# Performance work log

Measured on AMD Instinct MI355X. Metric: run time of the kernel, lower is better.

## Reference

```python
import jax, jax.numpy as jnp
import numpy as np

DIM = 256
H = 56
W = 56
WS = 7          # window_size
SHIFT = 3       # shift_size = WS // 2
NH = 8          # num_heads
HID = 4 * DIM   # mlp hidden
EPS = 1e-5
N = WS * WS     # tokens per window


def _rel_coords_table():
    # SwinV2 continuous log-spaced relative coords, pretrained_window_size=0
    r = np.arange(-(WS - 1), WS, dtype=np.float32)
    t = np.stack(np.meshgrid(r, r, indexing='ij'), axis=-1)[None]  # (1, 2WS-1, 2WS-1, 2)
    t = t / (WS - 1) * 8.0
    t = np.sign(t) * np.log2(np.abs(t) + 1.0) / np.log2(8.0)
    return jnp.asarray(t, jnp.float32)


def _rel_pos_index():
    coords = np.stack(np.meshgrid(np.arange(WS), np.arange(WS), indexing='ij'))  # (2, WS, WS)
    cf = coords.reshape(2, -1)
    rel = (cf[:, :, None] - cf[:, None, :]).transpose(1, 2, 0).astype(np.int64)  # (N, N, 2)
    rel[..., 0] += WS - 1
    rel[..., 1] += WS - 1
    rel[..., 0] *= 2 * WS - 1
    return jnp.asarray(rel.sum(-1), jnp.int32)  # (N, N)


def _attn_mask():
    # shifted-window mask: -100 where tokens come from different image regions
    img = np.zeros((1, H, W, 1), np.float32)
    cnt = 0
    for hs in (slice(0, -WS), slice(-WS, -SHIFT), slice(-SHIFT, None)):
        for ws_ in (slice(0, -WS), slice(-WS, -SHIFT), slice(-SHIFT, None)):
            img[:, hs, ws_, :] = cnt
            cnt += 1
    mw = img.reshape(1, H // WS, WS, W // WS, WS, 1).transpose(0, 1, 3, 2, 4, 5).reshape(-1, N)
    m = mw[:, None, :] - mw[:, :, None]
    return jnp.asarray(np.where(m != 0, -100.0, 0.0).astype(np.float32))  # (nW, N, N)


def _win_partition(x):  # (B, H, W, C) -> (B*nW, N, C)
    B, _, _, C = x.shape
    x = x.reshape(B, H // WS, WS, W // WS, WS, C).transpose(0, 1, 3, 2, 4, 5)
    return x.reshape(-1, N, C)


def _win_reverse(w, B):  # (B*nW, N, C) -> (B, H, W, C)
    C = w.shape[-1]
    x = w.reshape(B, H // WS, W // WS, WS, WS, C).transpose(0, 1, 3, 2, 4, 5)
    return x.reshape(B, H, W, C)


def _ln(x, g, b):
    mu = jnp.mean(x, axis=-1, keepdims=True)
    var = jnp.mean(jnp.square(x - mu), axis=-1, keepdims=True)
    return (x - mu) * jax.lax.rsqrt(var + EPS) * g + b


def setup_inputs() -> dict:
    key = jax.random.key(0)
    ks = jax.random.split(key, 16)
    s = lambda fan: 1.0 / np.sqrt(fan)
    return {
        'x': jax.random.normal(ks[0], (16, H * W, DIM), jnp.float32),
        'norm1_w': jnp.ones((DIM,), jnp.float32),
        'norm1_b': jnp.zeros((DIM,), jnp.float32),
        'qkv_w': jax.random.normal(ks[1], (3 * DIM, DIM), jnp.float32) * s(DIM),
        'q_bias': jnp.zeros((DIM,), jnp.float32),
        'v_bias': jnp.zeros((DIM,), jnp.float32),
        'logit_scale': jnp.full((NH, 1, 1), np.log(10.0), jnp.float32),
        'cpb_w1': jax.random.normal(ks[2], (512, 2), jnp.float32) * s(2),
        'cpb_b1': jnp.zeros((512,), jnp.float32),
        'cpb_w2': jax.random.normal(ks[3], (NH, 512), jnp.float32) * s(512),
        'proj_w': jax.random.normal(ks[4], (DIM, DIM), jnp.float32) * s(DIM),
        'proj_b': jnp.zeros((DIM,), jnp.float32),
        'norm2_w': jnp.ones((DIM,), jnp.float32),
        'norm2_b': jnp.zeros((DIM,), jnp.float32),
        'fc1_w': jax.random.normal(ks[5], (HID, DIM), jnp.float32) * s(DIM),
        'fc1_b': jnp.zeros((HID,), jnp.float32),
        'fc2_w': jax.random.normal(ks[6], (DIM, HID), jnp.float32) * s(HID),
        'fc2_b': jnp.zeros((DIM,), jnp.float32),
    }


def reference(x, norm1_w, norm1_b, qkv_w, q_bias, v_bias, logit_scale,
              cpb_w1, cpb_b1, cpb_w2, proj_w, proj_b,
              norm2_w, norm2_b, fc1_w, fc1_b, fc2_w, fc2_b):
    B, L, C = x.shape
    hd = C // NH
    shortcut = x

    # cyclic shift + window partition
    xs = jnp.roll(x.reshape(B, H, W, C), (-SHIFT, -SHIFT), axis=(1, 2))
    xw = _win_partition(xs)  # (B*nW, N, C)

    # qkv with q/v bias, zero k bias (SwinV2)
    qkv_b = jnp.concatenate([q_bias, jnp.zeros_like(q_bias), v_bias])
    qkv = (xw @ qkv_w.T + qkv_b).reshape(-1, N, 3, NH, hd).transpose(2, 0, 3, 1, 4)
    q, k, v = qkv[0], qkv[1], qkv[2]  # (B*nW, NH, N, hd)

    # cosine attention with clamped learned logit scale
    qn = q / jnp.maximum(jnp.linalg.norm(q, axis=-1, keepdims=True), 1e-12)
    kn = k / jnp.maximum(jnp.linalg.norm(k, axis=-1, keepdims=True), 1e-12)
    scale = jnp.exp(jnp.minimum(logit_scale, jnp.log(jnp.asarray(100.0, x.dtype))))
    attn = jnp.einsum('whnd,whmd->whnm', qn, kn) * scale[None]

    # continuous relative position bias via cpb MLP
    t = _rel_coords_table()  # (1, 2WS-1, 2WS-1, 2)
    tbl = (jax.nn.relu(t @ cpb_w1.T + cpb_b1) @ cpb_w2.T).reshape(-1, NH)
    rpb = tbl[_rel_pos_index().reshape(-1)].reshape(N, N, NH).transpose(2, 0, 1)
    attn = attn + (16.0 * jax.nn.sigmoid(rpb))[None]

    # shifted-window mask
    mask = _attn_mask()  # (nW, N, N)
    nW = mask.shape[0]
    attn = attn.reshape(B, nW, NH, N, N) + mask[None, :, None]
    attn = jax.nn.softmax(attn, axis=-1).reshape(-1, NH, N, N)

    out = jnp.einsum('whnm,whmd->whnd', attn, v).transpose(0, 2, 1, 3).reshape(-1, N, C)
    out = out @ proj_w.T + proj_b

    # reverse windows + reverse shift (SwinV2 post-norm residual)
    xs = jnp.roll(_win_reverse(out, B), (SHIFT, SHIFT), axis=(1, 2)).reshape(B, L, C)
    x = shortcut + _ln(xs, norm1_w, norm1_b)

    # MLP with tanh-approx GELU (matches Triton kernel), post-norm residual
    hmid = jax.nn.gelu(x @ fc1_w.T + fc1_b, approximate=True)
    mlp = hmid @ fc2_w.T + fc2_b
    return x + _ln(mlp, norm2_w, norm2_b)
```

## Files before the change

### kernel.cpp

```cpp
#include <hip/hip_runtime.h>
#include <hip/hip_bf16.h>

typedef __attribute__((ext_vector_type(8))) short short8;
typedef __attribute__((ext_vector_type(4))) float f32x4;

union I4S8 { int4 i; short8 s; };

#if defined(__has_builtin)
#if __has_builtin(__builtin_amdgcn_global_load_lds)
#define HAVE_GLL 1
#endif
#endif

__device__ __forceinline__ unsigned short f2b(float f) {
  union { __hip_bfloat16 h; unsigned short u; } c;
  c.h = __float2bfloat16(f);
  return c.u;
}
__device__ __forceinline__ unsigned pk2(float a, float b) {
  union { __hip_bfloat162 h2; unsigned u; } c;
  c.h2 = __hip_bfloat162{__float2bfloat16(a), __float2bfloat16(b)};
  return c.u;
}
__device__ __forceinline__ float b2f(unsigned short h) {
  return __uint_as_float(((unsigned)h) << 16);
}
__device__ __forceinline__ float gelu_fast(float v) {
  float c2 = 1.5957691216057308f * (v + 0.044715f * v * v * v);
  return v / (1.0f + __expf(-c2));
}

__device__ __forceinline__ void stage8(const unsigned short* ga, unsigned short* lds_base,
                                       int lane) {
#ifdef HAVE_GLL
  __builtin_amdgcn_global_load_lds(
      (const __attribute__((address_space(1))) void*)ga,
      (__attribute__((address_space(3))) void*)lds_base, 16, 0, 0);
#else
  *(int4*)(lds_base + (lane >> 3) * 64 + (lane & 7) * 8) = *(const int4*)ga;
#endif
}

__global__ void k_misc(const float* __restrict__ logit_scale,
                       const float* __restrict__ w1, const float* __restrict__ b1,
                       const float* __restrict__ w2,
                       float* __restrict__ scales, float* __restrict__ tblg) {
  const int bb = blockIdx.x;
  const int t = threadIdx.x;
  if (bb == 169) {
    if (t < 8) scales[t] = expf(fminf(logit_scale[t], logf(100.0f)));
    return;
  }
  __shared__ float red[4][8];
  int a = bb / 13, b = bb % 13;
  float ra = (float)(a - 6) * (8.0f / 6.0f);
  float rb = (float)(b - 6) * (8.0f / 6.0f);
  float sa = (ra > 0.f) ? 1.f : ((ra < 0.f) ? -1.f : 0.f);
  float sb = (rb > 0.f) ? 1.f : ((rb < 0.f) ? -1.f : 0.f);
  float t0 = sa * log2f(fabsf(ra) + 1.0f) / 3.0f;
  float t1 = sb * log2f(fabsf(rb) + 1.0f) / 3.0f;
  float acc[8];
#pragma unroll
  for (int hh = 0; hh < 8; ++hh) acc[hh] = 0.f;
#pragma unroll
  for (int jj = 0; jj < 2; ++jj) {
    int j = t + jj * 256;
    float hv = fmaxf(w1[2 * j] * t0 + w1[2 * j + 1] * t1 + b1[j], 0.0f);
#pragma unroll
    for (int hh = 0; hh < 8; ++hh) acc[hh] += w2[hh * 512 + j] * hv;
  }
#pragma unroll
  for (int hh = 0; hh < 8; ++hh) {
    acc[hh] += __shfl_xor(acc[hh], 1);
    acc[hh] += __shfl_xor(acc[hh], 2);
    acc[hh] += __shfl_xor(acc[hh], 4);
    acc[hh] += __shfl_xor(acc[hh], 8);
    acc[hh] += __shfl_xor(acc[hh], 16);
    acc[hh] += __shfl_xor(acc[hh], 32);
  }
  if ((t & 63) == 0) {
#pragma unroll
    for (int hh = 0; hh < 8; ++hh) red[t >> 6][hh] = acc[hh];
  }
  __syncthreads();
  if (t < 8) tblg[bb * 8 + t] = red[0][t] + red[1][t] + red[2][t] + red[3][t];
}

__global__ void k_bias(const float* __restrict__ tblg, float* __restrict__ biasT) {
  int idx = blockIdx.x * 256 + threadIdx.x;
  int h = idx >> 12, rem = idx & 4095, k = rem >> 6, q = rem & 63;
  float v;
  if (k >= 49 || q >= 49) {
    v = -3.0e8f;
  } else {
    int e = (q / 7 - k / 7 + 6) * 13 + (q % 7 - k % 7 + 6);
    float r = tblg[e * 8 + h];
    v = 16.0f / (1.0f + expf(-r));
  }
  biasT[idx] = v;
}

__global__ void k_cvt(const float* __restrict__ qkv_w, const float* __restrict__ proj_w,
                      const float* __restrict__ fc1_w, const float* __restrict__ fc2_w,
                      unsigned short* __restrict__ wq, unsigned short* __restrict__ wp,
                      unsigned short* __restrict__ w1, unsigned short* __restrict__ w2) {
  int i = blockIdx.x * 256 + threadIdx.x;
  if (i < 196608) wq[i] = f2b(qkv_w[i]);
  else if (i < 262144) wp[i - 196608] = f2b(proj_w[i - 196608]);
  else if (i < 524288) w1[i - 262144] = f2b(fc1_w[i - 262144]);
  else w2[i - 524288] = f2b(fc2_w[i - 524288]);
}

__global__ void k_xprep(const float* __restrict__ x, unsigned short* __restrict__ xw) {
  int id = blockIdx.x * 256 + threadIdx.x;
  int row = id >> 5, c8 = (id & 31) << 3;
  int win = row / 49, r = row - win * 49;
  int b = win >> 6, wi = (win >> 3) & 7, wj = win & 7;
  int i = r / 7, j = r - i * 7;
  int ho = (wi * 7 + i + 3) % 56;
  int wo = (wj * 7 + j + 3) % 56;
  const float* src = x + (size_t)(b * 3136 + ho * 56 + wo) * 256 + c8;
  float4 f0 = *(const float4*)(src);
  float4 f1 = *(const float4*)(src + 4);
  int4 pk;
  pk.x = pk2(f0.x, f0.y);
  pk.y = pk2(f0.z, f0.w);
  pk.z = pk2(f1.x, f1.y);
  pk.w = pk2(f1.z, f1.w);
  *(int4*)(xw + (size_t)row * 256 + c8) = pk;
}

__global__ void k_xb(const float* __restrict__ x1, unsigned short* __restrict__ xb) {
  int id = blockIdx.x * 256 + threadIdx.x;
  size_t off = (size_t)id << 3;
  const float* src = x1 + off;
  float4 f0 = *(const float4*)(src);
  float4 f1 = *(const float4*)(src + 4);
  int4 pk;
  pk.x = pk2(f0.x, f0.y);
  pk.y = pk2(f0.z, f0.w);
  pk.z = pk2(f1.x, f1.y);
  pk.w = pk2(f1.z, f1.w);
  *(int4*)(xb + off) = pk;
}

__launch_bounds__(512)
__global__ void k_qkvg(const unsigned short* __restrict__ xw, const unsigned short* __restrict__ wq,
                       const float* __restrict__ q_bias, const float* __restrict__ v_bias,
                       const float* __restrict__ scales, unsigned short* __restrict__ qkv) {
  const int mb = blockIdx.x, nb = blockIdx.y;
  const int t = threadIdx.x, lane = t & 63, w = t >> 6;
  const int wm = w >> 2, wn = w & 3;
  const int l15 = lane & 15, g = lane >> 4, rj = g << 2;

  __shared__ __align__(16) unsigned short As[128 * 64];
  __shared__ __align__(16) unsigned short Bs[256 * 64];

  f32x4 acc[4][4];
#pragma unroll
  for (int mf = 0; mf < 4; ++mf)
#pragma unroll
    for (int nf = 0; nf < 4; ++nf) acc[mf][nf] = (f32x4){0.f, 0.f, 0.f, 0.f};

  const int rl = lane >> 3;
  const int ca = (lane & 7) ^ rl;

  for (int kb = 0; kb < 4; ++kb) {
    __syncthreads();
#pragma unroll
    for (int i = 0; i < 6; ++i) {
      int gidx = w * 6 + i;
      if (gidx < 16) {
        int r = gidx * 8 + rl;
        stage8(xw + (size_t)(mb * 128 + r) * 256 + kb * 64 + ca * 8, As + gidx * 8 * 64, lane);
      } else {
        int gb = gidx - 16;
        int r = gb * 8 + rl;
        stage8(wq + (size_t)(nb * 256 + r) * 256 + kb * 64 + ca * 8, Bs + gb * 8 * 64, lane);
      }
    }
    __syncthreads();
#pragma unroll
    for (int ks = 0; ks < 2; ++ks) {
      short8 a_[4], b_[4];
#pragma unroll
      for (int mf = 0; mf < 4; ++mf) {
        int R = wm * 64 + mf * 16 + l15;
        a_[mf] = *(const short8*)(As + R * 64 + (((ks * 4 + g) ^ (R & 7)) << 3));
      }
#pragma unroll
      for (int nf = 0; nf < 4; ++nf) {
        int R = wn * 64 + nf * 16 + l15;
        b_[nf] = *(const short8*)(Bs + R * 64 + (((ks * 4 + g) ^ (R & 7)) << 3));
      }
#pragma unroll
      for (int mf = 0; mf < 4; ++mf)
#pragma unroll
        for (int nf = 0; nf < 4; ++nf)
          acc[mf][nf] = __builtin_amdgcn_mfma_f32_16x16x32_bf16(a_[mf], b_[nf], acc[mf][nf], 0, 0, 0);
    }
  }

  const int which = nb;
  if (which != 1) {
    const float* bp = (which == 0) ? q_bias : v_bias;
#pragma unroll
    for (int nf = 0; nf < 4; ++nf) {
      float bias = bp[wn * 64 + nf * 16 + l15];
#pragma unroll
      for (int mf = 0; mf < 4; ++mf)
#pragma unroll
        for (int j = 0; j < 4; ++j) acc[mf][nf][j] += bias;
    }
  }
  if (which < 2) {
#pragma unroll
    for (int mf = 0; mf < 4; ++mf)
#pragma unroll
      for (int p = 0; p < 2; ++p)
#pragma unroll
        for (int j = 0; j < 4; ++j) {
          float ss = acc[mf][2*p][j] * acc[mf][2*p][j] + acc[mf][2*p+1][j] * acc[mf][2*p+1][j];
          ss += __shfl_xor(ss, 1); ss += __shfl_xor(ss, 2);
          ss += __shfl_xor(ss, 4); ss += __shfl_xor(ss, 8);
          float inv = 1.0f / fmaxf(sqrtf(ss), 1e-12f);
          if (which == 0) inv *= scales[wn * 2 + p];
          acc[mf][2*p][j] *= inv;
          acc[mf][2*p+1][j] *= inv;
        }
  }
#pragma unroll
  for (int mf = 0; mf < 4; ++mf)
#pragma unroll
    for (int j = 0; j < 4; ++j) {
      int row_g = mb * 128 + wm * 64 + mf * 16 + rj + j;
      int win = row_g / 49, r = row_g - win * 49;
      size_t base = (((size_t)win * 3 + which) * 8) * 1568;
#pragma unroll
      for (int nf = 0; nf < 4; ++nf) {
        int h = wn * 2 + (nf >> 1), d = (nf & 1) * 16 + l15;
        qkv[base + (size_t)h * 1568 + r * 32 + d] = f2b(acc[mf][nf][j]);
      }
    }
}

__launch_bounds__(256, 4)
__global__ void k_attn2(unsigned short* __restrict__ qkv, const float* __restrict__ biasT) {
  const int win = blockIdx.x;
  const int wi = (win >> 3) & 7, wj = win & 7;
  const int t = threadIdx.x, lane = t & 63, w = t >> 6;
  const int l15 = lane & 15, g = lane >> 4;
  const int kk8 = g << 3, rj = g << 2;

  __shared__ __align__(16) unsigned short VT8[8 * 32 * 72];

  const int vi = (wi == 7) ? 1 : 0, vj = (wj == 7) ? 1 : 0;

  for (int idx = t; idx < 392; idx += 256) {
    int h = idx / 49, r = idx % 49;
    const unsigned short* vp = qkv + ((((size_t)win * 3 + 2) * 8 + h) * 49 + r) * 32;
    unsigned short vv[32];
    *(int4*)(vv + 0)  = *(const int4*)(vp + 0);
    *(int4*)(vv + 8)  = *(const int4*)(vp + 8);
    *(int4*)(vv + 16) = *(const int4*)(vp + 16);
    *(int4*)(vv + 24) = *(const int4*)(vp + 24);
    unsigned short* dst = VT8 + h * 2304;
#pragma unroll
    for (int d = 0; d < 32; ++d) dst[d * 72 + r] = vv[d];
  }
  for (int idx = t; idx < 3840; idx += 256) {
    int h = idx / 480, rem = idx % 480, d = rem / 15, r = 49 + rem % 15;
    VT8[h * 2304 + d * 72 + r] = 0;
  }
  __syncthreads();

  const int sA = l15 + ((g & 1) << 5);
  const int sB = sA + 16;
  const bool hi = ((g >> 1) & 1) != 0;

  unsigned ob[2][8][2];
  for (int hh = 0; hh < 2; ++hh) {
    const int h = w + hh * 4;
    const float* bT = biasT + (size_t)h * 4096;
    f32x4 s[4][4];
#pragma unroll
    for (int mf = 0; mf < 4; ++mf)
#pragma unroll
      for (int nf = 0; nf < 4; ++nf)
#pragma unroll
        for (int j = 0; j < 4; ++j)
          s[mf][nf][j] = bT[(mf * 16 + rj + j) * 64 + nf * 16 + l15];
    if (vi | vj) {
      int rq[4];
#pragma unroll
      for (int nf = 0; nf < 4; ++nf) {
        int q = nf * 16 + l15, qi = q / 7, qj = q - qi * 7;
        int aq = vi ? (qi < 4 ? 1 : 2) : 0;
        int bq = vj ? (qj < 4 ? 1 : 2) : 0;
        rq[nf] = aq * 3 + bq;
      }
#pragma unroll
      for (int mf = 0; mf < 4; ++mf)
#pragma unroll
        for (int j = 0; j < 4; ++j) {
          int k = mf * 16 + rj + j, ki = k / 7, kj = k - ki * 7;
          int ak = vi ? (ki < 4 ? 1 : 2) : 0;
          int bk = vj ? (kj < 4 ? 1 : 2) : 0;
          int rk = ak * 3 + bk;
#pragma unroll
          for (int nf = 0; nf < 4; ++nf)
            if (rq[nf] != rk) s[mf][nf][j] -= 100.0f;
        }
    }
    const unsigned short* kp = qkv + (((size_t)win * 3 + 1) * 8 + h) * 1568;
    const unsigned short* qp = qkv + (((size_t)win * 3 + 0) * 8 + h) * 1568;
    short8 ka[4], qa[4];
#pragma unroll
    for (int f = 0; f < 4; ++f) {
      ka[f] = *(const short8*)(kp + (f * 16 + l15) * 32 + kk8);
      qa[f] = *(const short8*)(qp + (f * 16 + l15) * 32 + kk8);
    }
#pragma unroll
    for (int mf = 0; mf < 4; ++mf)
#pragma unroll
      for (int nf = 0; nf < 4; ++nf)
        s[mf][nf] = __builtin_amdgcn_mfma_f32_16x16x32_bf16(ka[mf], qa[nf], s[mf][nf], 0, 0, 0);

    unsigned D[4][4][2];
#pragma unroll
    for (int nf = 0; nf < 4; ++nf) {
      float m = -3.0e8f;
#pragma unroll
      for (int mf = 0; mf < 4; ++mf)
#pragma unroll
        for (int j = 0; j < 4; ++j) m = fmaxf(m, s[mf][nf][j]);
      m = fmaxf(m, __shfl_xor(m, 16));
      m = fmaxf(m, __shfl_xor(m, 32));
      float sum = 0.f;
#pragma unroll
      for (int mf = 0; mf < 4; ++mf)
#pragma unroll
        for (int j = 0; j < 4; ++j) {
          float e = __expf(s[mf][nf][j] - m);
          s[mf][nf][j] = e; sum += e;
        }
      sum += __shfl_xor(sum, 16);
      sum += __shfl_xor(sum, 32);
      float inv = 1.0f / sum;
#pragma unroll
      for (int mf = 0; mf < 4; ++mf) {
        D[mf][nf][0] = pk2(s[mf][nf][0] * inv, s[mf][nf][1] * inv);
        D[mf][nf][1] = pk2(s[mf][nf][2] * inv, s[mf][nf][3] * inv);
      }
    }

    f32x4 o[8];
#pragma unroll
    for (int i = 0; i < 8; ++i) o[i] = (f32x4){0.f, 0.f, 0.f, 0.f};
#pragma unroll
    for (int ks = 0; ks < 2; ++ks) {
      short8 vb[2];
#pragma unroll
      for (int dt = 0; dt < 2; ++dt)
        vb[dt] = *(const short8*)(VT8 + h * 2304 + (dt * 16 + l15) * 72 + ks * 32 + kk8);
#pragma unroll
      for (int qt = 0; qt < 4; ++qt) {
        int a0 = __shfl((int)D[2*ks+0][qt][0], sA), a1 = __shfl((int)D[2*ks+1][qt][0], sA);
        int b0 = __shfl((int)D[2*ks+0][qt][1], sA), b1 = __shfl((int)D[2*ks+1][qt][1], sA);
        int c0 = __shfl((int)D[2*ks+0][qt][0], sB), c1 = __shfl((int)D[2*ks+1][qt][0], sB);
        int e0 = __shfl((int)D[2*ks+0][qt][1], sB), e1 = __shfl((int)D[2*ks+1][qt][1], sB);
        I4S8 u;
        u.i.x = hi ? a1 : a0;
        u.i.y = hi ? b1 : b0;
        u.i.z = hi ? c1 : c0;
        u.i.w = hi ? e1 : e0;
#pragma unroll
        for (int dt = 0; dt < 2; ++dt)
          o[qt * 2 + dt] = __builtin_amdgcn_mfma_f32_16x16x32_bf16(u.s, vb[dt], o[qt * 2 + dt], 0, 0, 0);
      }
    }
#pragma unroll
    for (int f = 0; f < 8; ++f) {
      ob[hh][f][0] = pk2(o[f][0], o[f][1]);
      ob[hh][f][1] = pk2(o[f][2], o[f][3]);
    }
  }
  __syncthreads();

  unsigned short* Ow = qkv + (size_t)win * 37632;
#pragma unroll
  for (int hh = 0; hh < 2; ++hh) {
    int h = w + hh * 4;
#pragma unroll
    for (int qt = 0; qt < 4; ++qt)
#pragma unroll
      for (int j = 0; j < 4; ++j) {
        int q = qt * 16 + rj + j;
        if (q < 49) {
#pragma unroll
          for (int dt = 0; dt < 2; ++dt)
            Ow[q * 256 + h * 32 + dt * 16 + l15] =
                (unsigned short)(ob[hh][qt * 2 + dt][j >> 1] >> ((j & 1) * 16));
        }
      }
  }
}

__launch_bounds__(256)
__global__ void k_proj(const unsigned short* __restrict__ qkvO, const unsigned short* __restrict__ wp,
                       const float* __restrict__ proj_b, const float* __restrict__ n1w,
                       const float* __restrict__ n1b, const float* __restrict__ x,
                       float* __restrict__ x1) {
  const int mb = blockIdx.x;
  const int t = threadIdx.x, lane = t & 63, w = t >> 6;
  const int l15 = lane & 15, g = lane >> 4, rj = g << 2;

  __shared__ __align__(16) unsigned short As[64 * 64];
  __shared__ __align__(16) unsigned short Bs[256 * 64];

  f32x4 acc[16];
#pragma unroll
  for (int nf = 0; nf < 16; ++nf) acc[nf] = (f32x4){0.f, 0.f, 0.f, 0.f};

  const int rl = lane >> 3;
  const int ca = (lane & 7) ^ rl;

  for (int kb = 0; kb < 4; ++kb) {
    __syncthreads();
#pragma unroll
    for (int cc = 0; cc < 2; ++cc) {
      int rloc = w * 16 + cc * 8 + rl;
      int row_g = mb * 64 + rloc;
      int win = row_g / 49, r = row_g - win * 49;
      stage8(qkvO + (size_t)win * 37632 + r * 256 + kb * 64 + ca * 8,
             As + (w * 16 + cc * 8) * 64, lane);
    }
#pragma unroll
    for (int cc = 0; cc < 4; ++cc) {
      int rloc = w * 64 + cc * 8 + rl;
      stage8(wp + (size_t)rloc * 256 + kb * 64 + ca * 8, Bs + (w * 64 + cc * 8) * 64, lane);
      int rloc2 = rloc + 32;
      stage8(wp + (size_t)rloc2 * 256 + kb * 64 + ca * 8, Bs + (w * 64 + cc * 8 + 32) * 64, lane);
    }
    __syncthreads();
#pragma unroll
    for (int ks = 0; ks < 2; ++ks) {
      int R = w * 16 + l15;
      short8 a_ = *(const short8*)(As + R * 64 + (((ks * 4 + g) ^ (R & 7)) << 3));
      short8 b_[16];
#pragma unroll
      for (int nf = 0; nf < 16; ++nf) {
        int Rb = nf * 16 + l15;
        b_[nf] = *(const short8*)(Bs + Rb * 64 + (((ks * 4 + g) ^ (Rb & 7)) << 3));
      }
#pragma unroll
      for (int nf = 0; nf < 16; ++nf)
        acc[nf] = __builtin_amdgcn_mfma_f32_16x16x32_bf16(a_, b_[nf], acc[nf], 0, 0, 0);
    }
  }
#pragma unroll
  for (int nf = 0; nf < 16; ++nf) {
    float bias = proj_b[nf * 16 + l15];
#pragma unroll
    for (int j = 0; j < 4; ++j) acc[nf][j] += bias;
  }
#pragma unroll
  for (int j = 0; j < 4; ++j) {
    float s = 0.f, s2 = 0.f;
#pragma unroll
    for (int nf = 0; nf < 16; ++nf) {
      float v = acc[nf][j];
      s += v; s2 += v * v;
    }
    s += __shfl_xor(s, 1);  s += __shfl_xor(s, 2);  s += __shfl_xor(s, 4);  s += __shfl_xor(s, 8);
    s2 += __shfl_xor(s2, 1); s2 += __shfl_xor(s2, 2); s2 += __shfl_xor(s2, 4); s2 += __shfl_xor(s2, 8);
    float mu = s * (1.0f / 256.0f);
    float var = s2 * (1.0f / 256.0f) - mu * mu;
    float rs = rsqrtf(var + 1e-5f);
    int row_g = mb * 64 + w * 16 + rj + j;
    int win = row_g / 49, r = row_g - win * 49;
    int b = win >> 6, wi = (win >> 3) & 7, wj = win & 7;
    int i2 = r / 7, j2 = r - i2 * 7;
    int ho = (wi * 7 + i2 + 3) % 56, wo = (wj * 7 + j2 + 3) % 56;
    size_t base = (size_t)(b * 3136 + ho * 56 + wo) * 256;
#pragma unroll
    for (int nf = 0; nf < 16; ++nf) {
      int col = nf * 16 + l15;
      float xv = x[base + col];
      x1[base + col] = xv + (acc[nf][j] - mu) * rs * n1w[col] + n1b[col];
    }
  }
}

__launch_bounds__(256)
__global__ void k_fc1(const unsigned short* __restrict__ xb, const unsigned short* __restrict__ w1,
                      const float* __restrict__ b1, unsigned short* __restrict__ Hbuf, int r0) {
  const int mb = blockIdx.x, nb = blockIdx.y;
  const int t = threadIdx.x, lane = t & 63, w = t >> 6;
  const int wm = w >> 1, wn = w & 1;
  const int l15 = lane & 15, g = lane >> 4, rj = g << 2;

  __shared__ __align__(16) char smem[36864];
  unsigned short* As = (unsigned short*)smem;
  unsigned short* Bs = (unsigned short*)(smem + 16384);
  unsigned short* Ct = (unsigned short*)smem;

  f32x4 acc[4][4];
#pragma unroll
  for (int mf = 0; mf < 4; ++mf)
#pragma unroll
    for (int nf = 0; nf < 4; ++nf) acc[mf][nf] = (f32x4){0.f, 0.f, 0.f, 0.f};

  const int row_g0 = r0 + mb * 128;
  const int rl = lane >> 3;
  const int ca = (lane & 7) ^ rl;

  for (int kb = 0; kb < 4; ++kb) {
    __syncthreads();
#pragma unroll
    for (int cc = 0; cc < 4; ++cc) {
      int r = w * 32 + cc * 8 + rl;
      stage8(xb + (size_t)(row_g0 + r) * 256 + kb * 64 + ca * 8, As + (w * 32 + cc * 8) * 64, lane);
      stage8(w1 + (size_t)(nb * 128 + r) * 256 + kb * 64 + ca * 8, Bs + (w * 32 + cc * 8) * 64, lane);
    }
    __syncthreads();
#pragma unroll
    for (int ks = 0; ks < 2; ++ks) {
      short8 a_[4], b_[4];
#pragma unroll
      for (int mf = 0; mf < 4; ++mf) {
        int R = wm * 64 + mf * 16 + l15;
        a_[mf] = *(const short8*)(As + R * 64 + (((ks * 4 + g) ^ (R & 7)) << 3));
      }
#pragma unroll
      for (int nf = 0; nf < 4; ++nf) {
        int R = wn * 64 + nf * 16 + l15;
        b_[nf] = *(const short8*)(Bs + R * 64 + (((ks * 4 + g) ^ (R & 7)) << 3));
      }
#pragma unroll
      for (int mf = 0; mf < 4; ++mf)
#pragma unroll
        for (int nf = 0; nf < 4; ++nf)
          acc[mf][nf] = __builtin_amdgcn_mfma_f32_16x16x32_bf16(a_[mf], b_[nf], acc[mf][nf], 0, 0, 0);
    }
  }
  __syncthreads();
#pragma unroll
  for (int mf = 0; mf < 4; ++mf)
#pragma unroll
    for (int nf = 0; nf < 4; ++nf) {
      float bias = b1[nb * 128 + wn * 64 + nf * 16 + l15];
#pragma unroll
      for (int j = 0; j < 4; ++j)
        Ct[(wm * 64 + mf * 16 + rj + j) * 138 + wn * 64 + nf * 16 + l15] =
            f2b(gelu_fast(acc[mf][nf][j] + bias));
    }
  __syncthreads();
  {
    int row = t >> 1, half = t & 1;
    const unsigned short* src = Ct + row * 138 + half * 64;
    unsigned short* dst = Hbuf + (size_t)(mb * 128 + row) * 1024 + nb * 128 + half * 64;
#pragma unroll
    for (int c = 0; c < 8; ++c)
      *(int4*)(dst + c * 8) = *(const int4*)(src + c * 8);
  }
}

__launch_bounds__(256)
__global__ void k_fc2(const unsigned short* __restrict__ Hbuf, const unsigned short* __restrict__ w2,
                      const float* __restrict__ b2, const float* __restrict__ n2w,
                      const float* __restrict__ n2b, float* __restrict__ xio, int r0) {
  const int mb = blockIdx.x;
  const int t = threadIdx.x, lane = t & 63, w = t >> 6;
  const int l15 = lane & 15, g = lane >> 4, rj = g << 2;

  __shared__ __align__(16) unsigned short As[64 * 64];
  __shared__ __align__(16) unsigned short Bs[256 * 64];

  f32x4 acc[16];
#pragma unroll
  for (int nf = 0; nf < 16; ++nf) acc[nf] = (f32x4){0.f, 0.f, 0.f, 0.f};

  const int rl = lane >> 3;
  const int ca = (lane & 7) ^ rl;

  for (int kb = 0; kb < 16; ++kb) {
    __syncthreads();
#pragma unroll
    for (int cc = 0; cc < 2; ++cc) {
      int rloc = w * 16 + cc * 8 + rl;
      stage8(Hbuf + (size_t)(mb * 64 + rloc) * 1024 + kb * 64 + ca * 8,
             As + (w * 16 + cc * 8) * 64, lane);
    }
#pragma unroll
    for (int cc = 0; cc < 4; ++cc) {
      int rloc = w * 64 + cc * 8 + rl;
      stage8(w2 + (size_t)rloc * 1024 + kb * 64 + ca * 8, Bs + (w * 64 + cc * 8) * 64, lane);
      int rloc2 = rloc + 32;
      stage8(w2 + (size_t)rloc2 * 1024 + kb * 64 + ca * 8, Bs + (w * 64 + cc * 8 + 32) * 64, lane);
    }
    __syncthreads();
#pragma unroll
    for (int ks = 0; ks < 2; ++ks) {
      int R = w * 16 + l15;
      short8 a_ = *(const short8*)(As + R * 64 + (((ks * 4 + g) ^ (R & 7)) << 3));
      short8 b_[16];
#pragma unroll
      for (int nf = 0; nf < 16; ++nf) {
        int Rb = nf * 16 + l15;
        b_[nf] = *(const short8*)(Bs + Rb * 64 + (((ks * 4 + g) ^ (Rb & 7)) << 3));
      }
#pragma unroll
      for (int nf = 0; nf < 16; ++nf)
        acc[nf] = __builtin_amdgcn_mfma_f32_16x16x32_bf16(a_, b_[nf], acc[nf], 0, 0, 0);
    }
  }
#pragma unroll
  for (int nf = 0; nf < 16; ++nf) {
    float bias = b2[nf * 16 + l15];
#pragma unroll
    for (int j = 0; j < 4; ++j) acc[nf][j] += bias;
  }
#pragma unroll
  for (int j = 0; j < 4; ++j) {
    float s = 0.f, s2 = 0.f;
#pragma unroll
    for (int nf = 0; nf < 16; ++nf) {
      float v = acc[nf][j];
      s += v; s2 += v * v;
    }
    s += __shfl_xor(s, 1);  s += __shfl_xor(s, 2);  s += __shfl_xor(s, 4);  s += __shfl_xor(s, 8);
    s2 += __shfl_xor(s2, 1); s2 += __shfl_xor(s2, 2); s2 += __shfl_xor(s2, 4); s2 += __shfl_xor(s2, 8);
    float mu = s * (1.0f / 256.0f);
    float var = s2 * (1.0f / 256.0f) - mu * mu;
    float rs = rsqrtf(var + 1e-5f);
    size_t base = (size_t)(r0 + mb * 64 + w * 16 + rj + j) * 256;
#pragma unroll
    for (int nf = 0; nf < 16; ++nf) {
      int col = nf * 16 + l15;
      float xv = xio[base + col];
      xio[base + col] = xv + (acc[nf][j] - mu) * rs * n2w[col] + n2b[col];
    }
  }
}

extern "C" void kernel_launch(void* const* d_in, const int* in_sizes, int n_in,
                              void* d_out, int out_size, void* d_ws, size_t ws_size,
                              hipStream_t stream) {
  const float* x           = (const float*)d_in[0];
  const float* norm1_w     = (const float*)d_in[1];
  const float* norm1_b     = (const float*)d_in[2];
  const float* qkv_w       = (const float*)d_in[3];
  const float* q_bias      = (const float*)d_in[4];
  const float* v_bias      = (const float*)d_in[5];
  const float* logit_scale = (const float*)d_in[6];
  const float* cpb_w1      = (const float*)d_in[7];
  const float* cpb_b1      = (const float*)d_in[8];
  const float* cpb_w2      = (const float*)d_in[9];
  const float* proj_w      = (const float*)d_in[10];
  const float* proj_b      = (const float*)d_in[11];
  const float* norm2_w     = (const float*)d_in[12];
  const float* norm2_b     = (const float*)d_in[13];
  const float* fc1_w       = (const float*)d_in[14];
  const float* fc1_b       = (const float*)d_in[15];
  const float* fc2_w       = (const float*)d_in[16];
  const float* fc2_b       = (const float*)d_in[17];

  char* ws = (char*)d_ws;
  float*          scales  = (float*)(ws + 0);
  float*          tblg    = (float*)(ws + 64);
  unsigned short* wq      = (unsigned short*)(ws + 8192);
  float*          biasT   = (float*)(ws + 8192);
  unsigned short* wp      = (unsigned short*)(ws + 401408);
  unsigned short* w1b     = (unsigned short*)(ws + 532480);
  unsigned short* w2b     = (unsigned short*)(ws + 1056768);
  unsigned short* qkvbuf  = (unsigned short*)(ws + 1581056);
  unsigned short* xb      = (unsigned short*)(ws + 1581056);
  unsigned short* Hbuf    = (unsigned short*)(ws + 27271168);
  float*          x1      = (float*)d_out;
  unsigned short* xw      = (unsigned short*)d_out;

  k_misc<<<dim3(170), dim3(256), 0, stream>>>(logit_scale, cpb_w1, cpb_b1, cpb_w2, scales, tblg);
  k_cvt<<<dim3(3072), dim3(256), 0, stream>>>(qkv_w, proj_w, fc1_w, fc2_w, wq, wp, w1b, w2b);
  k_xprep<<<dim3(6272), dim3(256), 0, stream>>>(x, xw);
  k_qkvg<<<dim3(392, 3), dim3(512), 0, stream>>>(xw, wq, q_bias, v_bias, scales, qkvbuf);
  k_bias<<<dim3(128), dim3(256), 0, stream>>>(tblg, biasT);
  k_attn2<<<dim3(1024), dim3(256), 0, stream>>>(qkvbuf, biasT);
  k_proj<<<dim3(784), dim3(256), 0, stream>>>(qkvbuf, wp, proj_b, norm1_w, norm1_b, x, x1);
  k_xb<<<dim3(6272), dim3(256), 0, stream>>>(x1, xb);
  k_fc1<<<dim3(196, 8), dim3(256), 0, stream>>>(xb, w1b, fc1_b, Hbuf, 0);
  k_fc2<<<dim3(392), dim3(256), 0, stream>>>(Hbuf, w2b, fc2_b, norm2_w, norm2_b, x1, 0);
  k_fc1<<<dim3(196, 8), dim3(256), 0, stream>>>(xb, w1b, fc1_b, Hbuf, 25088);
  k_fc2<<<dim3(392), dim3(256), 0, stream>>>(Hbuf, w2b, fc2_b, norm2_w, norm2_b, x1, 25088);
}
```

Baseline: 343.4 us.

## Store QKV as row-major planes via LDS-staged coalesced writes

Changes the QKV intermediate from per-window/per-head blocks to three row-major planes (Q, K, V) of tokens × 256 channels. The QKV GEMM epilogue now stages bf16 results through shared memory (reusing the A/B tile space) and writes full 16-byte vectors per row, replacing scattered 2-byte stores. The attention and projection kernels are updated to index the new layout, and the projection no longer needs a window/row division for its A loads. Attention Q/K reads now use a 512-byte row stride, which may be less contiguous per head.

```diff
diff --git a/kernel.cpp b/kernel.cpp
--- a/kernel.cpp
+++ b/kernel.cpp
@@ -11,6 +11,8 @@
 #define HAVE_GLL 1
 #endif
 #endif
+
+#define QKV_S 12845056
 
 __device__ __forceinline__ unsigned short f2b(float f) {
   union { __hip_bfloat16 h; unsigned short u; } c;
@@ -153,8 +155,10 @@
   const int wm = w >> 2, wn = w & 3;
   const int l15 = lane & 15, g = lane >> 4, rj = g << 2;
 
-  __shared__ __align__(16) unsigned short As[128 * 64];
-  __shared__ __align__(16) unsigned short Bs[256 * 64];
+  __shared__ __align__(16) char smem[49152];
+  unsigned short* As = (unsigned short*)smem;
+  unsigned short* Bs = (unsigned short*)(smem + 16384);
+  unsigned short* Ct = (unsigned short*)smem;
 
   f32x4 acc[4][4];
 #pragma unroll
@@ -229,19 +233,29 @@
           acc[mf][2*p+1][j] *= inv;
         }
   }
-#pragma unroll
-  for (int mf = 0; mf < 4; ++mf)
-#pragma unroll
-    for (int j = 0; j < 4; ++j) {
-      int row_g = mb * 128 + wm * 64 + mf * 16 + rj + j;
-      int win = row_g / 49, r = row_g - win * 49;
-      size_t base = (((size_t)win * 3 + which) * 8) * 1568;
-#pragma unroll
-      for (int nf = 0; nf < 4; ++nf) {
-        int h = wn * 2 + (nf >> 1), d = (nf & 1) * 16 + l15;
-        qkv[base + (size_t)h * 1568 + r * 32 + d] = f2b(acc[mf][nf][j]);
-      }
-    }
+  const size_t whichbase = (size_t)which * QKV_S;
+#pragma unroll
+  for (int half = 0; half < 2; ++half) {
+    __syncthreads();
+    if (wm == half) {
+#pragma unroll
+      for (int mf = 0; mf < 4; ++mf)
+#pragma unroll
+        for (int nf = 0; nf < 4; ++nf)
+#pragma unroll
+          for (int j = 0; j < 4; ++j)
+            Ct[(mf * 16 + rj + j) * 268 + wn * 64 + nf * 16 + l15] = f2b(acc[mf][nf][j]);
+    }
+    __syncthreads();
+    {
+      int row = t >> 3, seg = t & 7;
+      const unsigned short* src = Ct + row * 268 + seg * 32;
+      unsigned short* dst = qkv + whichbase + (size_t)(mb * 128 + half * 64 + row) * 256 + seg * 32;
+#pragma unroll
+      for (int c = 0; c < 4; ++c)
+        *(int4*)(dst + c * 8) = *(const int4*)(src + c * 8);
+    }
+  }
 }
 
 __launch_bounds__(256, 4)
@@ -255,10 +269,11 @@
   __shared__ __align__(16) unsigned short VT8[8 * 32 * 72];
 
   const int vi = (wi == 7) ? 1 : 0, vj = (wj == 7) ? 1 : 0;
+  const size_t rowbase = (size_t)win * 49 * 256;
 
   for (int idx = t; idx < 392; idx += 256) {
     int h = idx / 49, r = idx % 49;
-    const unsigned short* vp = qkv + ((((size_t)win * 3 + 2) * 8 + h) * 49 + r) * 32;
+    const unsigned short* vp = qkv + 2 * (size_t)QKV_S + rowbase + (size_t)r * 256 + h * 32;
     unsigned short vv[32];
     *(int4*)(vv + 0)  = *(const int4*)(vp + 0);
     *(int4*)(vv + 8)  = *(const int4*)(vp + 8);
@@ -312,13 +327,13 @@
             if (rq[nf] != rk) s[mf][nf][j] -= 100.0f;
         }
     }
-    const unsigned short* kp = qkv + (((size_t)win * 3 + 1) * 8 + h) * 1568;
-    const unsigned short* qp = qkv + (((size_t)win * 3 + 0) * 8 + h) * 1568;
+    const unsigned short* kp = qkv + (size_t)QKV_S + rowbase + h * 32;
+    const unsigned short* qp = qkv + rowbase + h * 32;
     short8 ka[4], qa[4];
 #pragma unroll
     for (int f = 0; f < 4; ++f) {
-      ka[f] = *(const short8*)(kp + (f * 16 + l15) * 32 + kk8);
-      qa[f] = *(const short8*)(qp + (f * 16 + l15) * 32 + kk8);
+      ka[f] = *(const short8*)(kp + (size_t)(f * 16 + l15) * 256 + kk8);
+      qa[f] = *(const short8*)(qp + (size_t)(f * 16 + l15) * 256 + kk8);
     }
 #pragma unroll
     for (int mf = 0; mf < 4; ++mf)
@@ -387,7 +402,7 @@
   }
   __syncthreads();
 
-  unsigned short* Ow = qkv + (size_t)win * 37632;
+  unsigned short* Ow = qkv + rowbase;
 #pragma unroll
   for (int hh = 0; hh < 2; ++hh) {
     int h = w + hh * 4;
@@ -399,7 +414,7 @@
         if (q < 49) {
 #pragma unroll
           for (int dt = 0; dt < 2; ++dt)
-            Ow[q * 256 + h * 32 + dt * 16 + l15] =
+            Ow[(size_t)q * 256 + h * 32 + dt * 16 + l15] =
                 (unsigned short)(ob[hh][qt * 2 + dt][j >> 1] >> ((j & 1) * 16));
         }
       }
@@ -430,9 +445,7 @@
 #pragma unroll
     for (int cc = 0; cc < 2; ++cc) {
       int rloc = w * 16 + cc * 8 + rl;
-      int row_g = mb * 64 + rloc;
-      int win = row_g / 49, r = row_g - win * 49;
-      stage8(qkvO + (size_t)win * 37632 + r * 256 + kb * 64 + ca * 8,
+      stage8(qkvO + (size_t)(mb * 64 + rloc) * 256 + kb * 64 + ca * 8,
              As + (w * 16 + cc * 8) * 64, lane);
     }
 #pragma unroll
```

Result: slower. 369.8 us (+7.7%).
